# Performance work log

Hardware: AMD Instinct MI355X
Metric: run time of the kernel (lower is better)

## Reference

```python
import jax, jax.numpy as jnp
import numpy as np

B, L_IN, F = 64, 256, 64
N_EXO = 16
N_ENDO = F - N_EXO
H = 1024
L_OUT = 64


def _lstm_params(key, in_dim, hid):
    k = 1.0 / np.sqrt(hid)
    k1, k2, k3, k4 = jax.random.split(key, 4)
    Wih = jax.random.uniform(k1, (4 * hid, in_dim), jnp.float32, -k, k)
    Whh = jax.random.uniform(k2, (4 * hid, hid), jnp.float32, -k, k)
    bih = jax.random.uniform(k3, (4 * hid,), jnp.float32, -k, k)
    bhh = jax.random.uniform(k4, (4 * hid,), jnp.float32, -k, k)
    return Wih, Whh, bih, bhh


def setup_inputs() -> dict:
    key = jax.random.key(0)
    ks = jax.random.split(key, 8)
    src = jax.random.normal(ks[0], (B, L_IN, F), jnp.float32)
    trg = jax.random.normal(ks[1], (B, L_OUT, F), jnp.float32)
    eW0 = _lstm_params(ks[2], F, H)
    eW1 = _lstm_params(ks[3], H, H)
    dW0 = _lstm_params(ks[4], F, H)  # decoder input size = n_endo + n_exo = F
    dW1 = _lstm_params(ks[5], H, H)
    kf = 1.0 / np.sqrt(H)
    fc_W = jax.random.uniform(ks[6], (N_ENDO, H), jnp.float32, -kf, kf)
    fc_b = jax.random.uniform(ks[7], (N_ENDO,), jnp.float32, -kf, kf)
    return {
        'src': src, 'trg': trg,
        'enc_Wih0': eW0[0], 'enc_Whh0': eW0[1], 'enc_bih0': eW0[2], 'enc_bhh0': eW0[3],
        'enc_Wih1': eW1[0], 'enc_Whh1': eW1[1], 'enc_bih1': eW1[2], 'enc_bhh1': eW1[3],
        'dec_Wih0': dW0[0], 'dec_Whh0': dW0[1], 'dec_bih0': dW0[2], 'dec_bhh0': dW0[3],
        'dec_Wih1': dW1[0], 'dec_Whh1': dW1[1], 'dec_bih1': dW1[2], 'dec_bhh1': dW1[3],
        'fc_W': fc_W, 'fc_b': fc_b,
    }


def _cell(x, h, c, Wih, Whh, bih, bhh):
    # torch gate order: i, f, g, o
    gates = x @ Wih.T + h @ Whh.T + (bih + bhh)
    i, f, g, o = jnp.split(gates, 4, axis=-1)
    c_new = jax.nn.sigmoid(f) * c + jax.nn.sigmoid(i) * jnp.tanh(g)
    h_new = jax.nn.sigmoid(o) * jnp.tanh(c_new)
    return h_new, c_new


def reference(src, trg,
              enc_Wih0, enc_Whh0, enc_bih0, enc_bhh0,
              enc_Wih1, enc_Whh1, enc_bih1, enc_bhh1,
              dec_Wih0, dec_Whh0, dec_bih0, dec_bhh0,
              dec_Wih1, dec_Whh1, dec_bih1, dec_bhh1,
              fc_W, fc_b):
    b = src.shape[0]
    z = jnp.zeros((b, H), src.dtype)

    # ---- encoder: 2-layer LSTM over src time dim ----
    def enc_step(carry, x_t):
        h0, c0, h1, c1 = carry
        h0, c0 = _cell(x_t, h0, c0, enc_Wih0, enc_Whh0, enc_bih0, enc_bhh0)
        h1, c1 = _cell(h0, h1, c1, enc_Wih1, enc_Whh1, enc_bih1, enc_bhh1)
        return (h0, c0, h1, c1), None

    (h0, c0, h1, c1), _ = jax.lax.scan(enc_step, (z, z, z, z),
                                       jnp.swapaxes(src, 0, 1))  # [L_in, B, F]

    exo = jnp.swapaxes(trg[:, :, N_ENDO:], 0, 1)  # [L_out, B, n_exo]
    dec_in0 = src[:, -1, :]

    def dec_step(carry, exo_t):
        h0, c0, h1, c1, x = carry
        h0, c0 = _cell(x, h0, c0, dec_Wih0, dec_Whh0, dec_bih0, dec_bhh0)
        h1, c1 = _cell(h0, h1, c1, dec_Wih1, dec_Whh1, dec_bih1, dec_bhh1)
        pred = h1 @ fc_W.T + fc_b  # [B, n_endo]
        x_next = jnp.concatenate([pred, exo_t], axis=1)
        return (h0, c0, h1, c1, x_next), pred

    _, preds = jax.lax.scan(dec_step, (h0, c0, h1, c1, dec_in0), exo)
    return jnp.swapaxes(preds, 0, 1)  # [B, L_out, n_endo]
```

## Files before the change

### kernel.cpp

```cpp
#include <hip/hip_runtime.h>
#include <math.h>

#define LIN 256
#define LOUT 64
#define NENDO 48

typedef __attribute__((ext_vector_type(8))) short short8;
typedef __attribute__((ext_vector_type(4))) float f32x4;
typedef __attribute__((ext_vector_type(16))) float f32x16;

constexpr size_t O_APE0 = 0;
constexpr size_t O_APE1 = 17825792;
constexpr size_t O_APD0 = 51380224;
constexpr size_t O_APD1 = 69206016;
constexpr size_t O_SRCF = 102760448;
constexpr size_t O_EXH  = 106954752;
constexpr size_t O_EXL  = 107085824;
constexpr size_t O_H0F  = 107216896;
constexpr size_t O_H1F  = 107741184;
constexpr size_t O_XF   = 108265472;
constexpr size_t O_H1KM = 108298240;
constexpr size_t O_BIAS = 108560384;
constexpr size_t O_BAR  = 108625920;

#define IB_ARR(j)  ((j) * 64)
#define IB_EPC  512
#define IB_EPF  576
#define IB_SLOT(x) (640 + (x) * 64)
#define IB_DONE(x) (1216 + (x) * 64)
#define SPIN_GUARD (1 << 20)

__device__ __forceinline__ unsigned short f2bh(float x) {
    unsigned int u = __float_as_uint(x);
    unsigned int r = (u + 0x7fffu + ((u >> 16) & 1u)) >> 16;
    return (unsigned short)r;
}
__device__ __forceinline__ float bh2f(unsigned short h) {
    return __uint_as_float(((unsigned int)h) << 16);
}
__device__ __forceinline__ float sigf(float x) { return 1.0f / (1.0f + expf(-x)); }

__device__ __forceinline__ void store_us_cc(unsigned short* p, unsigned short v) {
    unsigned int w = v;
    asm volatile("global_store_short %0, %1, off sc0 sc1" :: "v"(p), "v"(w) : "memory");
}
__device__ __forceinline__ void store_f_cc(float* p, float v) {
    asm volatile("global_store_dword %0, %1, off sc0 sc1" :: "v"(p), "v"(v) : "memory");
}

__device__ __forceinline__ void load4_c0(const unsigned short* base,
                                         short8& h0, short8& l0, short8& h1, short8& l1)
{
    asm volatile(
        "global_load_dwordx4 %0, %4, off sc0\n\t"
        "global_load_dwordx4 %1, %4, off offset:1024 sc0\n\t"
        "global_load_dwordx4 %2, %4, off offset:2048 sc0\n\t"
        "global_load_dwordx4 %3, %4, off offset:3072 sc0"
        : "=&v"(h0), "=&v"(l0), "=&v"(h1), "=&v"(l1)
        : "v"(base)
        : "memory");
}
__device__ __forceinline__ void load_f_c0_issue(const float* p, float& dst) {
    asm volatile("global_load_dword %0, %1, off sc0" : "=v"(dst) : "v"(p) : "memory");
}

__device__ __forceinline__ int get_xcc_id() {
    int x;
    asm("s_getreg_b32 %0, hwreg(HW_REG_XCC_ID)" : "=s"(x));
    return x & 7;
}

__device__ __forceinline__ size_t frag_off(int k, int b, int spl) {
    return (size_t)(k >> 4) * 2048 + (size_t)(b >> 5) * 1024 + (size_t)spl * 512
         + (size_t)((b & 31) + 32 * ((k >> 3) & 1)) * 8 + (k & 7);
}

__global__ void pack_a32(const float* __restrict__ Wx, const float* __restrict__ Wh,
                         unsigned short* __restrict__ out, int KX, int NC)
{
    const int n = 128 * NC * 512;
    for (int j = blockIdx.x * blockDim.x + threadIdx.x; j < n; j += gridDim.x * blockDim.x) {
        int r2 = j & 511;
        int c = (j >> 9) % NC;
        int T = (j >> 9) / NC;
        int l = r2 >> 3, e = r2 & 7;
        int p = T * 32 + (l & 31);
        int hcol = p >> 2, gate = p & 3;
        int k = c * 16 + (l >> 5) * 8 + e;
        float v = (k < KX) ? Wx[(gate * 1024 + hcol) * KX + k]
                           : Wh[(gate * 1024 + hcol) * 1024 + (k - KX)];
        unsigned short h = f2bh(v);
        size_t o = ((size_t)(T * NC + c) * 2) * 512 + r2;
        out[o] = h;
        out[o + 512] = f2bh(v - bh2f(h));
    }
}

__global__ void pack_bias_kernel(const float* a0, const float* b0, const float* a1, const float* b1,
                                 const float* a2, const float* b2, const float* a3, const float* b3,
                                 float* d)
{
    int i = blockIdx.x * blockDim.x + threadIdx.x;
    if (i >= 4096) return;
    int hcol = i >> 2, gate = i & 3, s = (gate << 10) + hcol;
    d[i] = a0[s] + b0[s];
    d[4096 + i] = a1[s] + b1[s];
    d[8192 + i] = a2[s] + b2[s];
    d[12288 + i] = a3[s] + b3[s];
}

__global__ void prep_misc(const float* __restrict__ src, const float* __restrict__ trg,
                          char* __restrict__ wsb)
{
    unsigned short* hz = (unsigned short*)(wsb + O_H0F);
    int* bar = (int*)(wsb + O_BAR);
    unsigned short* srcf = (unsigned short*)(wsb + O_SRCF);
    unsigned short* exh = (unsigned short*)(wsb + O_EXH);
    unsigned short* exl = (unsigned short*)(wsb + O_EXL);
    unsigned short* xf0 = (unsigned short*)(wsb + O_XF);
    const int N0 = 524288, N1 = 2048, N2 = 1048576, N3 = 65536, N4 = 4096;
    const int TOT = N0 + N1 + N2 + N3 + N4;
    for (int i = blockIdx.x * blockDim.x + threadIdx.x; i < TOT; i += gridDim.x * blockDim.x) {
        if (i < N0) {
            hz[i] = 0;
        } else if (i < N0 + N1) {
            bar[i - N0] = 0;
        } else if (i < N0 + N1 + N2) {
            int j = i - (N0 + N1);
            int t = j >> 12, b = (j >> 6) & 63, k = j & 63;
            float v = src[(b * LIN + t) * 64 + k];
            unsigned short h = f2bh(v);
            unsigned short* d = srcf + (size_t)t * 8192;
            d[frag_off(k, b, 0)] = h;
            d[frag_off(k, b, 1)] = f2bh(v - bh2f(h));
        } else if (i < N0 + N1 + N2 + N3) {
            int j = i - (N0 + N1 + N2);
            int t = j >> 10, b = (j >> 4) & 63, e = j & 15;
            float v = trg[(b * LOUT + t) * 64 + NENDO + e];
            unsigned short h = f2bh(v);
            exh[j] = h; exl[j] = f2bh(v - bh2f(h));
        } else {
            int j = i - (N0 + N1 + N2 + N3);
            int b = j >> 6, k = j & 63;
            float v = src[(b * LIN + (LIN - 1)) * 64 + k];
            unsigned short h = f2bh(v);
            xf0[frag_off(k, b, 0)] = h;
            xf0[frag_off(k, b, 1)] = f2bh(v - bh2f(h));
        }
    }
}

template <int CNT>
__device__ __forceinline__ void load_a(const unsigned short* __restrict__ ap, int T, int NC,
                                       int base, int l, short8* A)
{
#pragma unroll
    for (int i = 0; i < CNT; i++) {
#pragma unroll
        for (int s = 0; s < 2; s++)
            A[i * 2 + s] = *(const short8*)(ap + (((size_t)T * NC + (base + i)) * 2 + s) * 512 + l * 8);
    }
}

template <int CNT>
__device__ __forceinline__ void compute_ph(const unsigned short* __restrict__ B1, int S,
                                           const unsigned short* __restrict__ B2,
                                           int base, const short8* A, int l,
                                           f32x16& a0, f32x16& a1)
{
    short8 bh0[2], bl0[2], bh1[2], bl1[2];
    auto addr = [&](int i) -> const unsigned short* {
        int ks = base + i;
        const unsigned short* fb = (ks < S) ? (B1 + (size_t)ks * 2048) : (B2 + (size_t)(ks - S) * 2048);
        return fb + l * 8;
    };
    load4_c0(addr(0), bh0[0], bl0[0], bh1[0], bl1[0]);
    __builtin_amdgcn_sched_barrier(0);
#pragma unroll
    for (int i = 0; i < CNT; i++) {
        const int cur = i & 1, nxt = cur ^ 1;
        if (i + 1 < CNT) {
            load4_c0(addr(i + 1), bh0[nxt], bl0[nxt], bh1[nxt], bl1[nxt]);
            __builtin_amdgcn_sched_barrier(0);
            asm volatile("s_waitcnt vmcnt(4)" ::: "memory");
        } else {
            asm volatile("s_waitcnt vmcnt(0)" ::: "memory");
        }
        __builtin_amdgcn_sched_barrier(0);
        short8 ah = A[i * 2], al = A[i * 2 + 1];
        a0 = __builtin_amdgcn_mfma_f32_32x32x16_bf16(ah, bh0[cur], a0, 0, 0, 0);
        a1 = __builtin_amdgcn_mfma_f32_32x32x16_bf16(ah, bh1[cur], a1, 0, 0, 0);
        a0 = __builtin_amdgcn_mfma_f32_32x32x16_bf16(ah, bl0[cur], a0, 0, 0, 0);
        a1 = __builtin_amdgcn_mfma_f32_32x32x16_bf16(ah, bl1[cur], a1, 0, 0, 0);
        a0 = __builtin_amdgcn_mfma_f32_32x32x16_bf16(al, bh0[cur], a0, 0, 0, 0);
        a1 = __builtin_amdgcn_mfma_f32_32x32x16_bf16(al, bh1[cur], a1, 0, 0, 0);
        __builtin_amdgcn_sched_barrier(0);
    }
}

__device__ __forceinline__ void reduce_epi(float* ldsf, f32x16& a0, f32x16& a1,
                                           int w, int l, int T,
                                           const float* __restrict__ biasP,
                                           unsigned short* __restrict__ Hout,
                                           float* __restrict__ km, float* creg)
{
    const int l31 = l & 31, l5 = l >> 5;
    __syncthreads();
#pragma unroll
    for (int j = 0; j < 16; j++) {
        ldsf[((w * 2 + 0) * 16 + j) * 64 + l] = a0[j];
        ldsf[((w * 2 + 1) * 16 + j) * 64 + l] = a1[j];
    }
    __syncthreads();
    if (w < 2) {
#pragma unroll
        for (int q = 0; q < 4; q++) {
            float gv[4];
#pragma unroll
            for (int j = 0; j < 4; j++) {
                float v = 0.0f;
#pragma unroll
                for (int kt = 0; kt < 8; kt++) v += ldsf[((kt * 2 + w) * 16 + (q * 4 + j)) * 64 + l];
                gv[j] = v;
            }
            int hcol = T * 8 + 2 * q + l5;
            int b = w * 32 + l31;
            const f32x4 bv = *(const f32x4*)(biasP + hcol * 4);
            float ig = sigf(gv[0] + bv[0]);
            float fg = sigf(gv[1] + bv[1]);
            float gg = tanhf(gv[2] + bv[2]);
            float og = sigf(gv[3] + bv[3]);
            float cv = fg * creg[q] + ig * gg;
            creg[q] = cv;
            float hv = og * tanhf(cv);
            if (km) store_f_cc(km + hcol * 64 + b, hv);
            unsigned short hh = f2bh(hv);
            unsigned short hl = f2bh(hv - bh2f(hh));
            size_t fo = (size_t)(T >> 1) * 2048 + (size_t)w * 1024
                      + (size_t)(l31 + 32 * (T & 1)) * 8 + (2 * q + l5);
            store_us_cc(Hout + fo, hh);
            store_us_cc(Hout + fo + 512, hl);
        }
    }
}

__device__ __forceinline__ void gridbar(int* bar, int& ep, int tid, int grp)
{
    asm volatile("s_waitcnt vmcnt(0)" ::: "memory");
    __syncthreads();
    ep++;
    if (tid == 0) {
        int a = __hip_atomic_fetch_add(&bar[IB_ARR(grp)], 1, __ATOMIC_RELAXED, __HIP_MEMORY_SCOPE_AGENT);
        if (a == ep * 32 - 1) {
            int g2 = __hip_atomic_fetch_add(&bar[IB_EPC], 1, __ATOMIC_RELAXED, __HIP_MEMORY_SCOPE_AGENT);
            if (g2 == ep * 8 - 1)
                __hip_atomic_store(&bar[IB_EPF], ep, __ATOMIC_RELAXED, __HIP_MEMORY_SCOPE_AGENT);
        }
        int gu = 0;
        while (__hip_atomic_load(&bar[IB_EPF], __ATOMIC_RELAXED, __HIP_MEMORY_SCOPE_AGENT) < ep) {
            __builtin_amdgcn_s_sleep(1);
            if (++gu > SPIN_GUARD) break;
        }
        const int xcd = get_xcc_id();
        int old = __hip_atomic_fetch_max(&bar[IB_SLOT(xcd)], ep, __ATOMIC_RELAXED, __HIP_MEMORY_SCOPE_AGENT);
        if (old < ep) {
            __builtin_amdgcn_fence(__ATOMIC_ACQUIRE, "agent");
            asm volatile("s_waitcnt vmcnt(0)" ::: "memory");
            __hip_atomic_store(&bar[IB_DONE(xcd)], ep, __ATOMIC_RELAXED, __HIP_MEMORY_SCOPE_AGENT);
        } else {
            int gu2 = 0;
            while (__hip_atomic_load(&bar[IB_DONE(xcd)], __ATOMIC_RELAXED, __HIP_MEMORY_SCOPE_AGENT) < ep) {
                __builtin_amdgcn_s_sleep(1);
                if (++gu2 > SPIN_GUARD) break;
            }
        }
    }
    __syncthreads();
}

__global__ __launch_bounds__(512, 2) void persist(char* __restrict__ wsb,
                                                  const float* __restrict__ fcW,
                                                  const float* __restrict__ fcb,
                                                  float* __restrict__ out)
{
    __shared__ float ldsf[16384];

    const unsigned short* apE0 = (const unsigned short*)(wsb + O_APE0);
    const unsigned short* apE1 = (const unsigned short*)(wsb + O_APE1);
    const unsigned short* apD0 = (const unsigned short*)(wsb + O_APD0);
    const unsigned short* apD1 = (const unsigned short*)(wsb + O_APD1);
    const unsigned short* srcf = (const unsigned short*)(wsb + O_SRCF);
    const unsigned short* exh = (const unsigned short*)(wsb + O_EXH);
    const unsigned short* exl = (const unsigned short*)(wsb + O_EXL);
    unsigned short* h0f[2] = { (unsigned short*)(wsb + O_H0F), (unsigned short*)(wsb + O_H0F + 262144) };
    unsigned short* h1f[2] = { (unsigned short*)(wsb + O_H1F), (unsigned short*)(wsb + O_H1F + 262144) };
    unsigned short* xf[2] = { (unsigned short*)(wsb + O_XF), (unsigned short*)(wsb + O_XF + 16384) };
    float* h1km = (float*)(wsb + O_H1KM);
    const float* biasB = (const float*)(wsb + O_BIAS);
    int* bar = (int*)(wsb + O_BAR);

    const int tid = threadIdx.x;
    const int l = tid & 63;
    const int w = tid >> 6;
    const int g = blockIdx.x;
    const int grp = g >> 5;
    const bool isL0 = g < 128;
    const int T = isL0 ? g : g - 128;
    const int base0 = (w < 4) ? w * 9 : 36 + (w - 4) * 8;
    int ep = 0;

    short8 Areg[32];
    float creg[4] = {0.f, 0.f, 0.f, 0.f};

    if (isL0) {
        if (w < 4) load_a<9>(apE0, T, 68, base0, l, Areg);
        else       load_a<8>(apE0, T, 68, base0, l, Areg);
    } else {
        load_a<16>(apE1, T, 128, w * 16, l, Areg);
    }

    for (int d = 0; d <= LIN; d++) {
        if (isL0) {
            if (d < LIN) {
                f32x16 a0 = {}, a1 = {};
                const unsigned short* B1 = srcf + (size_t)d * 8192;
                const unsigned short* B2 = h0f[(d + 1) & 1];
                if (w < 4) compute_ph<9>(B1, 4, B2, base0, Areg, l, a0, a1);
                else       compute_ph<8>(B1, 4, B2, base0, Areg, l, a0, a1);
                reduce_epi(ldsf, a0, a1, w, l, T, biasB, h0f[d & 1], nullptr, creg);
            }
        } else {
            if (d >= 1) {
                f32x16 a0 = {}, a1 = {};
                const unsigned short* B1 = h0f[(d + 1) & 1];
                const unsigned short* B2 = h1f[(d + 1) & 1];
                compute_ph<16>(B1, 64, B2, w * 16, Areg, l, a0, a1);
                reduce_epi(ldsf, a0, a1, w, l, T, biasB + 4096, h1f[d & 1], nullptr, creg);
            }
        }
        gridbar(bar, ep, tid, grp);
    }

    if (isL0) {
        if (w < 4) load_a<9>(apD0, T, 68, base0, l, Areg);
        else       load_a<8>(apD0, T, 68, base0, l, Areg);
    } else {
        load_a<16>(apD1, T, 128, w * 16, l, Areg);
    }

    for (int t = 0; t < LOUT; t++) {
        if (isL0) {
            f32x16 a0 = {}, a1 = {};
            const unsigned short* B1 = xf[t & 1];
            const unsigned short* B2 = h0f[(t + 1) & 1];
            if (w < 4) compute_ph<9>(B1, 4, B2, base0, Areg, l, a0, a1);
            else       compute_ph<8>(B1, 4, B2, base0, Areg, l, a0, a1);
            reduce_epi(ldsf, a0, a1, w, l, T, biasB + 8192, h0f[t & 1], nullptr, creg);
        }
        gridbar(bar, ep, tid, grp);

        if (!isL0) {
            f32x16 a0 = {}, a1 = {};
            const unsigned short* B1 = h0f[t & 1];
            const unsigned short* B2 = h1f[t & 1];
            compute_ph<16>(B1, 64, B2, w * 16, Areg, l, a0, a1);
            reduce_epi(ldsf, a0, a1, w, l, T, biasB + 12288, h1f[(t + 1) & 1], h1km, creg);
        }
        gridbar(bar, ep, tid, grp);

        if (g < NENDO) {
            const int b_ = tid & 63, kw = tid >> 6;
            const float* hp = h1km + b_;
            const float* wp = fcW + g * 1024 + kw * 128;
            float vb[2][32];
            float acc = 0.0f;
#pragma unroll
            for (int u = 0; u < 32; u++)
                load_f_c0_issue(hp + (size_t)(kw * 128 + u) * 64, vb[0][u]);
            __builtin_amdgcn_sched_barrier(0);
#pragma unroll
            for (int j = 0; j < 4; j++) {
                if (j + 1 < 4) {
#pragma unroll
                    for (int u = 0; u < 32; u++)
                        load_f_c0_issue(hp + (size_t)(kw * 128 + (j + 1) * 32 + u) * 64, vb[(j + 1) & 1][u]);
                    __builtin_amdgcn_sched_barrier(0);
                    asm volatile("s_waitcnt vmcnt(32)" ::: "memory");
                } else {
                    asm volatile("s_waitcnt vmcnt(0)" ::: "memory");
                }
                __builtin_amdgcn_sched_barrier(0);
#pragma unroll
                for (int u = 0; u < 32; u++)
                    acc = fmaf(vb[j & 1][u], wp[j * 32 + u], acc);
            }
            __syncthreads();
            ldsf[kw * 64 + b_] = acc;
            __syncthreads();
            if (tid < 64) {
                float s = fcb[g];
#pragma unroll
                for (int j = 0; j < 8; j++) s += ldsf[j * 64 + tid];
                store_f_cc(out + tid * (LOUT * NENDO) + t * NENDO + g, s);
                unsigned short hh = f2bh(s);
                unsigned short hl = f2bh(s - bh2f(hh));
                unsigned short* x2 = xf[(t + 1) & 1];
                store_us_cc(x2 + frag_off(g, tid, 0), hh);
                store_us_cc(x2 + frag_off(g, tid, 1), hl);
            }
        } else if (g == NENDO) {
#pragma unroll
            for (int r = 0; r < 2; r++) {
                int idx = tid + r * 512;
                int e = idx >> 6, b = idx & 63;
                int k = NENDO + e;
                unsigned short* x2 = xf[(t + 1) & 1];
                store_us_cc(x2 + frag_off(k, b, 0), exh[t * 1024 + b * 16 + e]);
                store_us_cc(x2 + frag_off(k, b, 1), exl[t * 1024 + b * 16 + e]);
            }
        }
        gridbar(bar, ep, tid, grp);
    }
}

extern "C" void kernel_launch(void* const* d_in, const int* in_sizes, int n_in,
                              void* d_out, int out_size, void* d_ws, size_t ws_size,
                              hipStream_t stream)
{
    const float* src = (const float*)d_in[0];
    const float* trg = (const float*)d_in[1];
    const float* eWih0 = (const float*)d_in[2];
    const float* eWhh0 = (const float*)d_in[3];
    const float* ebih0 = (const float*)d_in[4];
    const float* ebhh0 = (const float*)d_in[5];
    const float* eWih1 = (const float*)d_in[6];
    const float* eWhh1 = (const float*)d_in[7];
    const float* ebih1 = (const float*)d_in[8];
    const float* ebhh1 = (const float*)d_in[9];
    const float* dWih0 = (const float*)d_in[10];
    const float* dWhh0 = (const float*)d_in[11];
    const float* dbih0 = (const float*)d_in[12];
    const float* dbhh0 = (const float*)d_in[13];
    const float* dWih1 = (const float*)d_in[14];
    const float* dWhh1 = (const float*)d_in[15];
    const float* dbih1 = (const float*)d_in[16];
    const float* dbhh1 = (const float*)d_in[17];
    const float* fcW = (const float*)d_in[18];
    const float* fcb = (const float*)d_in[19];

    char* wsb = (char*)d_ws;
    float* out = (float*)d_out;
    auto U = [&](size_t o) { return (unsigned short*)(wsb + o); };

    pack_a32<<<2048, 256, 0, stream>>>(eWih0, eWhh0, U(O_APE0), 64, 68);
    pack_a32<<<4096, 256, 0, stream>>>(eWih1, eWhh1, U(O_APE1), 1024, 128);
    pack_a32<<<2048, 256, 0, stream>>>(dWih0, dWhh0, U(O_APD0), 64, 68);
    pack_a32<<<4096, 256, 0, stream>>>(dWih1, dWhh1, U(O_APD1), 1024, 128);
    pack_bias_kernel<<<16, 256, 0, stream>>>(ebih0, ebhh0, ebih1, ebhh1,
                                             dbih0, dbhh0, dbih1, dbhh1,
                                             (float*)(wsb + O_BIAS));
    prep_misc<<<1024, 256, 0, stream>>>(src, trg, wsb);

    persist<<<256, 512, 0, stream>>>(wsb, fcW, fcb, out);
}
```

Baseline: 7.702 ms.

## Group grid barrier by XCD with leader-only polling and deepen B prefetch

The grid barrier now groups blocks by their physical XCC ID, counted at kernel start, instead of by block-index groups of 32. Only the last-arriving block of each XCD polls the global epoch flag and then releases its XCD-local done flag, so fewer blocks poll the shared global word. The MFMA inner loop also keeps four B-fragment loads in flight instead of two, to hide more memory latency. This costs more registers and adds a one-time startup barrier to count blocks per XCD.

After: 8.341 ms. +8.3%, slower.

```diff
diff --git a/kernel.cpp b/kernel.cpp
--- a/kernel.cpp
+++ b/kernel.cpp
@@ -23,11 +23,14 @@
 constexpr size_t O_BIAS = 108560384;
 constexpr size_t O_BAR  = 108625920;
 
-#define IB_ARR(j)  ((j) * 64)
+#define IB_ARR(x)  ((x) * 64)
 #define IB_EPC  512
 #define IB_EPF  576
-#define IB_SLOT(x) (640 + (x) * 64)
-#define IB_DONE(x) (1216 + (x) * 64)
+#define IB_DONE(x) (640 + (x) * 64)
+#define IB_G0   1216
+#define IB_GF   1280
+#define IB_CNT(x)  (1344 + (x) * 64)
+#define IB_NX   1920
 #define SPIN_GUARD (1 << 20)
 
 __device__ __forceinline__ unsigned short f2bh(float x) {
@@ -62,6 +65,15 @@
 }
 __device__ __forceinline__ void load_f_c0_issue(const float* p, float& dst) {
     asm volatile("global_load_dword %0, %1, off sc0" : "=v"(dst) : "v"(p) : "memory");
+}
+
+__device__ __forceinline__ void wait_vm(int n) {
+    switch (n) {
+    case 0:  asm volatile("s_waitcnt vmcnt(0)"  ::: "memory"); break;
+    case 4:  asm volatile("s_waitcnt vmcnt(4)"  ::: "memory"); break;
+    case 8:  asm volatile("s_waitcnt vmcnt(8)"  ::: "memory"); break;
+    default: asm volatile("s_waitcnt vmcnt(12)" ::: "memory"); break;
+    }
 }
 
 __device__ __forceinline__ int get_xcc_id() {
@@ -168,33 +180,35 @@
                                            int base, const short8* A, int l,
                                            f32x16& a0, f32x16& a1)
 {
-    short8 bh0[2], bl0[2], bh1[2], bl1[2];
+    constexpr int D = 4;
+    short8 bh0[D], bl0[D], bh1[D], bl1[D];
     auto addr = [&](int i) -> const unsigned short* {
         int ks = base + i;
         const unsigned short* fb = (ks < S) ? (B1 + (size_t)ks * 2048) : (B2 + (size_t)(ks - S) * 2048);
         return fb + l * 8;
     };
-    load4_c0(addr(0), bh0[0], bl0[0], bh1[0], bl1[0]);
+#pragma unroll
+    for (int i = 0; i < D; i++)
+        load4_c0(addr(i), bh0[i], bl0[i], bh1[i], bl1[i]);
     __builtin_amdgcn_sched_barrier(0);
 #pragma unroll
     for (int i = 0; i < CNT; i++) {
-        const int cur = i & 1, nxt = cur ^ 1;
-        if (i + 1 < CNT) {
-            load4_c0(addr(i + 1), bh0[nxt], bl0[nxt], bh1[nxt], bl1[nxt]);
-            __builtin_amdgcn_sched_barrier(0);
-            asm volatile("s_waitcnt vmcnt(4)" ::: "memory");
-        } else {
-            asm volatile("s_waitcnt vmcnt(0)" ::: "memory");
-        }
+        const int slot = i % D;
+        const int rem = CNT - 1 - i;
+        wait_vm(4 * (rem < D - 1 ? rem : D - 1));
         __builtin_amdgcn_sched_barrier(0);
         short8 ah = A[i * 2], al = A[i * 2 + 1];
-        a0 = __builtin_amdgcn_mfma_f32_32x32x16_bf16(ah, bh0[cur], a0, 0, 0, 0);
-        a1 = __builtin_amdgcn_mfma_f32_32x32x16_bf16(ah, bh1[cur], a1, 0, 0, 0);
-        a0 = __builtin_amdgcn_mfma_f32_32x32x16_bf16(ah, bl0[cur], a0, 0, 0, 0);
-        a1 = __builtin_amdgcn_mfma_f32_32x32x16_bf16(ah, bl1[cur], a1, 0, 0, 0);
-        a0 = __builtin_amdgcn_mfma_f32_32x32x16_bf16(al, bh0[cur], a0, 0, 0, 0);
-        a1 = __builtin_amdgcn_mfma_f32_32x32x16_bf16(al, bh1[cur], a1, 0, 0, 0);
+        a0 = __builtin_amdgcn_mfma_f32_32x32x16_bf16(ah, bh0[slot], a0, 0, 0, 0);
+        a1 = __builtin_amdgcn_mfma_f32_32x32x16_bf16(ah, bh1[slot], a1, 0, 0, 0);
+        a0 = __builtin_amdgcn_mfma_f32_32x32x16_bf16(ah, bl0[slot], a0, 0, 0, 0);
+        a1 = __builtin_amdgcn_mfma_f32_32x32x16_bf16(ah, bl1[slot], a1, 0, 0, 0);
+        a0 = __builtin_amdgcn_mfma_f32_32x32x16_bf16(al, bh0[slot], a0, 0, 0, 0);
+        a1 = __builtin_amdgcn_mfma_f32_32x32x16_bf16(al, bh1[slot], a1, 0, 0, 0);
         __builtin_amdgcn_sched_barrier(0);
+        if (i + D < CNT) {
+            load4_c0(addr(i + D), bh0[slot], bl0[slot], bh1[slot], bl1[slot]);
+            __builtin_amdgcn_sched_barrier(0);
+        }
     }
 }
 
@@ -244,34 +258,30 @@
     }
 }
 
-__device__ __forceinline__ void gridbar(int* bar, int& ep, int tid, int grp)
+__device__ __forceinline__ void gridbar(int* bar, int& ep, int tid, int xcd, int cntx, int nx)
 {
     asm volatile("s_waitcnt vmcnt(0)" ::: "memory");
     __syncthreads();
     ep++;
     if (tid == 0) {
-        int a = __hip_atomic_fetch_add(&bar[IB_ARR(grp)], 1, __ATOMIC_RELAXED, __HIP_MEMORY_SCOPE_AGENT);
-        if (a == ep * 32 - 1) {
+        int a = __hip_atomic_fetch_add(&bar[IB_ARR(xcd)], 1, __ATOMIC_RELAXED, __HIP_MEMORY_SCOPE_AGENT);
+        if (a == ep * cntx - 1) {
             int g2 = __hip_atomic_fetch_add(&bar[IB_EPC], 1, __ATOMIC_RELAXED, __HIP_MEMORY_SCOPE_AGENT);
-            if (g2 == ep * 8 - 1)
+            if (g2 == ep * nx - 1)
                 __hip_atomic_store(&bar[IB_EPF], ep, __ATOMIC_RELAXED, __HIP_MEMORY_SCOPE_AGENT);
-        }
-        int gu = 0;
-        while (__hip_atomic_load(&bar[IB_EPF], __ATOMIC_RELAXED, __HIP_MEMORY_SCOPE_AGENT) < ep) {
-            __builtin_amdgcn_s_sleep(1);
-            if (++gu > SPIN_GUARD) break;
-        }
-        const int xcd = get_xcc_id();
-        int old = __hip_atomic_fetch_max(&bar[IB_SLOT(xcd)], ep, __ATOMIC_RELAXED, __HIP_MEMORY_SCOPE_AGENT);
-        if (old < ep) {
+            int gu = 0;
+            while (__hip_atomic_load(&bar[IB_EPF], __ATOMIC_RELAXED, __HIP_MEMORY_SCOPE_AGENT) < ep) {
+                __builtin_amdgcn_s_sleep(1);
+                if (++gu > SPIN_GUARD) break;
+            }
             __builtin_amdgcn_fence(__ATOMIC_ACQUIRE, "agent");
             asm volatile("s_waitcnt vmcnt(0)" ::: "memory");
             __hip_atomic_store(&bar[IB_DONE(xcd)], ep, __ATOMIC_RELAXED, __HIP_MEMORY_SCOPE_AGENT);
         } else {
-            int gu2 = 0;
+            int gu = 0;
             while (__hip_atomic_load(&bar[IB_DONE(xcd)], __ATOMIC_RELAXED, __HIP_MEMORY_SCOPE_AGENT) < ep) {
                 __builtin_amdgcn_s_sleep(1);
-                if (++gu2 > SPIN_GUARD) break;
+                if (++gu > SPIN_GUARD) break;
             }
         }
     }
@@ -284,6 +294,7 @@
                                                   float* __restrict__ out)
 {
     __shared__ float ldsf[16384];
+    __shared__ int sbc[3];
 
     const unsigned short* apE0 = (const unsigned short*)(wsb + O_APE0);
     const unsigned short* apE1 = (const unsigned short*)(wsb + O_APE1);
@@ -303,11 +314,30 @@
     const int l = tid & 63;
     const int w = tid >> 6;
     const int g = blockIdx.x;
-    const int grp = g >> 5;
     const bool isL0 = g < 128;
     const int T = isL0 ? g : g - 128;
     const int base0 = (w < 4) ? w * 9 : 36 + (w - 4) * 8;
     int ep = 0;
+
+    if (tid == 0) {
+        int xcd = get_xcc_id();
+        int c = __hip_atomic_fetch_add(&bar[IB_CNT(xcd)], 1, __ATOMIC_RELAXED, __HIP_MEMORY_SCOPE_AGENT);
+        if (c == 0)
+            __hip_atomic_fetch_add(&bar[IB_NX], 1, __ATOMIC_RELAXED, __HIP_MEMORY_SCOPE_AGENT);
+        int a = __hip_atomic_fetch_add(&bar[IB_G0], 1, __ATOMIC_RELAXED, __HIP_MEMORY_SCOPE_AGENT);
+        if (a == 255)
+            __hip_atomic_store(&bar[IB_GF], 1, __ATOMIC_RELAXED, __HIP_MEMORY_SCOPE_AGENT);
+        int gu = 0;
+        while (__hip_atomic_load(&bar[IB_GF], __ATOMIC_RELAXED, __HIP_MEMORY_SCOPE_AGENT) < 1) {
+            __builtin_amdgcn_s_sleep(2);
+            if (++gu > SPIN_GUARD) break;
+        }
+        sbc[0] = __hip_atomic_load(&bar[IB_CNT(xcd)], __ATOMIC_RELAXED, __HIP_MEMORY_SCOPE_AGENT);
+        sbc[1] = __hip_atomic_load(&bar[IB_NX], __ATOMIC_RELAXED, __HIP_MEMORY_SCOPE_AGENT);
+        sbc[2] = xcd;
+    }
+    __syncthreads();
+    const int cntx = sbc[0], nx = sbc[1], xcd = sbc[2];
 
     short8 Areg[32];
     float creg[4] = {0.f, 0.f, 0.f, 0.f};
@@ -338,7 +368,7 @@
                 reduce_epi(ldsf, a0, a1, w, l, T, biasB + 4096, h1f[d & 1], nullptr, creg);
             }
         }
-        gridbar(bar, ep, tid, grp);
+        gridbar(bar, ep, tid, xcd, cntx, nx);
     }
 
     if (isL0) {
@@ -357,7 +387,7 @@
             else       compute_ph<8>(B1, 4, B2, base0, Areg, l, a0, a1);
             reduce_epi(ldsf, a0, a1, w, l, T, biasB + 8192, h0f[t & 1], nullptr, creg);
         }
-        gridbar(bar, ep, tid, grp);
+        gridbar(bar, ep, tid, xcd, cntx, nx);
 
         if (!isL0) {
             f32x16 a0 = {}, a1 = {};
@@ -366,7 +396,7 @@
             compute_ph<16>(B1, 64, B2, w * 16, Areg, l, a0, a1);
             reduce_epi(ldsf, a0, a1, w, l, T, biasB + 12288, h1f[(t + 1) & 1], h1km, creg);
         }
-        gridbar(bar, ep, tid, grp);
+        gridbar(bar, ep, tid, xcd, cntx, nx);
 
         if (g < NENDO) {
             const int b_ = tid & 63, kw = tid >> 6;
@@ -419,7 +449,7 @@
                 store_us_cc(x2 + frag_off(k, b, 1), exl[t * 1024 + b * 16 + e]);
             }
         }
-        gridbar(bar, ep, tid, grp);
+        gridbar(bar, ep, tid, xcd, cntx, nx);
     }
 }
 
```
